# Performance work log

Hardware: AMD Instinct MI355X
Metric: run time of the kernel (lower is better)

The kernel has to match this reference:

```python
import jax, jax.numpy as jnp
import numpy as np

B, L, D, H = 4, 2048, 1024, 16
HD = D // H


def setup_inputs() -> dict:
    key = jax.random.key(0)
    k0, k1, k2, k3, k4 = jax.random.split(key, 5)
    scale = 1.0 / np.sqrt(D)
    x = jax.random.normal(k0, (B, L, D), dtype=jnp.float32)
    Wk = jax.random.normal(k1, (D, D), dtype=jnp.float32) * scale
    Wv = jax.random.normal(k2, (D, D), dtype=jnp.float32) * scale
    Wr = jax.random.normal(k3, (D, D), dtype=jnp.float32) * scale
    Wo = jax.random.normal(k4, (D, D), dtype=jnp.float32) * scale
    # time_decay init: geometric decay per head, broadcast over head_dim
    decay = jnp.exp(-5.0 * jnp.arange(1, H + 1, dtype=jnp.float32) / H)
    time_decay = jnp.broadcast_to(decay[:, None], (H, HD)).astype(jnp.float32)
    time_first = jnp.full((H, HD), 0.5, dtype=jnp.float32)
    return {"x": x, "Wk": Wk, "Wv": Wv, "Wr": Wr, "Wo": Wo,
            "time_decay": time_decay, "time_first": time_first}


def reference(x, Wk, Wv, Wr, Wo, time_decay, time_first):
    b, l, d = x.shape
    h, hd = time_decay.shape
    # projections (nn.Linear: x @ W.T)
    k = (x @ Wk.T).reshape(b, l, h, hd)
    v = (x @ Wv.T).reshape(b, l, h, hd)
    r = jax.nn.sigmoid(x @ Wr.T).reshape(b, l, h, hd)

    decay = time_decay[None, :, :, None]   # (1,H,HD,1) broadcast over 'e' axis
    tf = time_first[None, :, :, None]      # (1,H,HD,1)

    def step(state, inp):
        k_t, v_t, r_t = inp                 # each (B,H,HD)
        # state: (B,H,HD,HD); outer product k_t (d) x v_t (e)
        state = state * decay + (k_t[..., :, None] * v_t[..., None, :]) * tf
        y_t = jnp.einsum('bhde,bhd->bhe', state, r_t)
        return state, y_t

    state0 = jnp.zeros((b, h, hd, hd), dtype=x.dtype)
    seq = (jnp.moveaxis(k, 1, 0), jnp.moveaxis(v, 1, 0), jnp.moveaxis(r, 1, 0))
    final_state, ys = jax.lax.scan(step, state0, seq)   # ys: (L,B,H,HD)
    y = jnp.moveaxis(ys, 0, 1).reshape(b, l, d) @ Wo.T
    return y, final_state
```

## Files before the change

### kernel.cpp

```cpp
#include <hip/hip_runtime.h>

typedef unsigned short u16;
typedef unsigned int   u32;
typedef __attribute__((ext_vector_type(8))) short bfrag;
typedef __attribute__((ext_vector_type(4))) float ffrag;

#define MFMA16(a,b,c) __builtin_amdgcn_mfma_f32_16x16x32_bf16((a),(b),(c),0,0,0)

#define GLL16(gp, lp) __builtin_amdgcn_global_load_lds( \
    (const __attribute__((address_space(1))) u32*)(gp), \
    (__attribute__((address_space(3))) u32*)(lp), 16, 0, 0)

__device__ __forceinline__ u16 f2b(float f) {
  u32 u = __float_as_uint(f);
  return (u16)((u + 0x7fffu + ((u >> 16) & 1u)) >> 16);
}
__device__ __forceinline__ float b2f(u16 v) { return __uint_as_float(((u32)v) << 16); }

__device__ __forceinline__ void unpack8(uint4 q, u16 e[8]) {
  e[0] = q.x & 0xffffu; e[1] = q.x >> 16;
  e[2] = q.y & 0xffffu; e[3] = q.y >> 16;
  e[4] = q.z & 0xffffu; e[5] = q.z >> 16;
  e[6] = q.w & 0xffffu; e[7] = q.w >> 16;
}

__device__ __forceinline__ bfrag scale_frag(bfrag a, float s) {
  u16* p = (u16*)&a;
  bfrag r;
  u16* q = (u16*)&r;
#pragma unroll
  for (int j = 0; j < 8; ++j) q[j] = f2b(b2f(p[j]) * s);
  return r;
}

__global__ __launch_bounds__(256) void cvt_all(
    const float* __restrict__ x,  const float* __restrict__ wk,
    const float* __restrict__ wv, const float* __restrict__ wr,
    const float* __restrict__ wo,
    u16* __restrict__ xb, u16* __restrict__ wb, u16* __restrict__ wob)
{
  size_t i4 = ((size_t)blockIdx.x * 256 + threadIdx.x) * 4;
  const float* src; u16* dst; size_t off;
  if      (i4 <  8388608) { src = x;  dst = xb;            off = i4; }
  else if (i4 <  9437184) { src = wk; dst = wb;            off = i4 - 8388608; }
  else if (i4 < 10485760) { src = wv; dst = wb + 1048576;  off = i4 - 9437184; }
  else if (i4 < 11534336) { src = wr; dst = wb + 2097152;  off = i4 - 10485760; }
  else                    { src = wo; dst = wob;           off = i4 - 11534336; }
  float4 f = *(const float4*)(src + off);
  u16 o[4] = { f2b(f.x), f2b(f.y), f2b(f.z), f2b(f.w) };
  *(ushort4*)(dst + off) = make_ushort4(o[0], o[1], o[2], o[3]);
}

__global__ __launch_bounds__(256) void k1_proj(
    const u16* __restrict__ xb, const u16* __restrict__ wb,
    const float* __restrict__ tf,
    u16* __restrict__ kws, u16* __restrict__ vws, u16* __restrict__ rws)
{
  __shared__ u16 As[2][128 * 32];
  __shared__ u16 Bs[2][128 * 32];
  const int tid  = threadIdx.x;
  const int wave = tid >> 6, lane = tid & 63;
  const int li = lane & 15, quad = lane >> 4;
  const int wr = (wave >> 1) * 64, wc = (wave & 1) * 64;

  const int bid = blockIdx.x;
  const int xcd = bid & 7, lb = bid >> 3;
  const int n0 = (xcd * 3 + (lb % 3)) * 128;
  const int m0 = (lb / 3) * 128;

  ffrag acc[4][4];
#pragma unroll
  for (int i = 0; i < 4; ++i)
#pragma unroll
    for (int j = 0; j < 4; ++j)
#pragma unroll
      for (int r = 0; r < 4; ++r) acc[i][j][r] = 0.f;

  const int srow = wave * 16 + (lane >> 2);
  const int scol = (lane & 3) * 8;

  for (int kk = 0; kk < 1024; kk += 64) {
    const u16* ga = xb + (size_t)(m0 + srow) * 1024 + kk + scol;
    const u16* gb = wb + (size_t)(n0 + srow) * 1024 + kk + scol;
    GLL16(ga,                  As[0] + wave * 512);
    GLL16(ga + 64 * 1024,      As[0] + 2048 + wave * 512);
    GLL16(ga + 32,             As[1] + wave * 512);
    GLL16(ga + 32 + 64 * 1024, As[1] + 2048 + wave * 512);
    GLL16(gb,                  Bs[0] + wave * 512);
    GLL16(gb + 64 * 1024,      Bs[0] + 2048 + wave * 512);
    GLL16(gb + 32,             Bs[1] + wave * 512);
    GLL16(gb + 32 + 64 * 1024, Bs[1] + 2048 + wave * 512);
    __syncthreads();

#pragma unroll
    for (int h2 = 0; h2 < 2; ++h2) {
      bfrag av[4], bv[4];
#pragma unroll
      for (int i = 0; i < 4; ++i) av[i] = *(const bfrag*)&As[h2][(wr + i * 16 + li) * 32 + quad * 8];
#pragma unroll
      for (int j = 0; j < 4; ++j) bv[j] = *(const bfrag*)&Bs[h2][(wc + j * 16 + li) * 32 + quad * 8];
#pragma unroll
      for (int i = 0; i < 4; ++i)
#pragma unroll
        for (int j = 0; j < 4; ++j)
          acc[i][j] = MFMA16(av[i], bv[j], acc[i][j]);
    }
    __syncthreads();
  }

  const int sel = n0 >> 10;
#pragma unroll
  for (int i = 0; i < 4; ++i) {
#pragma unroll
    for (int j = 0; j < 4; ++j) {
#pragma unroll
      for (int r = 0; r < 4; ++r) {
        int m = m0 + wr + i * 16 + quad * 4 + r;
        int n = n0 + wc + j * 16 + li;
        int c = n & 1023;
        int bb = m >> 11, l = m & 2047;
        size_t dst = (size_t)((bb << 4) | (c >> 6)) * 131072 + (size_t)l * 64 + (c & 63);
        float v = acc[i][j][r];
        if (sel == 0)      kws[dst] = f2b(v * tf[c]);
        else if (sel == 1) vws[dst] = f2b(v);
        else               rws[dst] = f2b(1.f / (1.f + __expf(-v)));
      }
    }
  }
}

#define ST 72

__global__ __launch_bounds__(256) void k2a_u(
    const u16* __restrict__ kws, const u16* __restrict__ vws,
    const float* __restrict__ td, float* __restrict__ ut)
{
  __shared__ u16 KbarT[64 * ST];
  __shared__ u16 Vt[64 * ST];
  const int tid = threadIdx.x;
  const int lane = tid & 63, wave = tid >> 6;
  const int li = lane & 15, quad = lane >> 4;
  const int wr = (wave >> 1) * 32, wc = (wave & 1) * 32;
  const int bid = blockIdx.x;
  const int bh = bid >> 5, ch = bid & 31;
  const int h = bh & 15;
  const float l2D = log2f(td[h * 64]);
  const size_t base = (size_t)bh * 131072 + (size_t)ch * 4096;

#pragma unroll
  for (int it = 0; it < 2; ++it) {
    int c16 = tid + it * 256;
    int row = c16 >> 3, c8 = (c16 & 7) * 8;
    size_t g = base + (size_t)row * 64 + c8;
    uint4 kq = *(const uint4*)(kws + g);
    u16 ke[8]; unpack8(kq, ke);
    float sk = exp2f((float)(63 - row) * l2D);
#pragma unroll
    for (int j = 0; j < 8; ++j) KbarT[(c8 + j) * ST + row] = f2b(b2f(ke[j]) * sk);
    uint4 vq = *(const uint4*)(vws + g);
    u16 ve[8]; unpack8(vq, ve);
#pragma unroll
    for (int j = 0; j < 8; ++j) Vt[(c8 + j) * ST + row] = ve[j];
  }
  __syncthreads();

  ffrag U[2][2];
#pragma unroll
  for (int a = 0; a < 2; ++a)
#pragma unroll
    for (int b = 0; b < 2; ++b)
#pragma unroll
      for (int r = 0; r < 4; ++r) U[a][b][r] = 0.f;
#pragma unroll
  for (int kk = 0; kk < 64; kk += 32) {
    bfrag a0 = *(const bfrag*)&Vt[(wr + li) * ST + kk + quad * 8];
    bfrag a1 = *(const bfrag*)&Vt[(wr + 16 + li) * ST + kk + quad * 8];
    bfrag b0 = *(const bfrag*)&KbarT[(wc + li) * ST + kk + quad * 8];
    bfrag b1 = *(const bfrag*)&KbarT[(wc + 16 + li) * ST + kk + quad * 8];
    U[0][0] = MFMA16(a0, b0, U[0][0]);
    U[0][1] = MFMA16(a0, b1, U[0][1]);
    U[1][0] = MFMA16(a1, b0, U[1][0]);
    U[1][1] = MFMA16(a1, b1, U[1][1]);
  }

  float* dst = ut + ((size_t)bid << 12);
#pragma unroll
  for (int ti = 0; ti < 2; ++ti)
#pragma unroll
    for (int tj = 0; tj < 2; ++tj)
#pragma unroll
      for (int r = 0; r < 4; ++r) {
        int e = wr + ti * 16 + quad * 4 + r;
        int d = wc + tj * 16 + li;
        dst[e * 64 + d] = U[ti][tj][r];
      }
}

__global__ __launch_bounds__(256) void k2b_scan(
    const float* __restrict__ ut, const float* __restrict__ td,
    u16* __restrict__ sbf, float* __restrict__ fstate)
{
  __shared__ float Sl[4 * 65];
  const int tid = threadIdx.x;
  const int bid = blockIdx.x;
  const int bh = bid >> 4, q = bid & 15;
  const int ed = q * 256 + tid;
  const int h = bh & 15;
  const float Dh = td[h * 64];
  const float DhC = exp2f(64.f * log2f(Dh));

  float S = 0.f;
  size_t idx = ((size_t)bh * 32) * 4096 + ed;
  for (int c = 0; c < 32; ++c, idx += 4096) {
    sbf[idx] = f2b(S);
    S = S * DhC + ut[idx];
  }
  Sl[(tid >> 6) * 65 + (tid & 63)] = S;
  __syncthreads();
  int d = tid >> 2, el = tid & 3;
  fstate[(size_t)bh * 4096 + (size_t)d * 64 + q * 4 + el] = Sl[el * 65 + d];
}

__global__ __launch_bounds__(256) void k2c_y(
    const u16* __restrict__ kws, const u16* __restrict__ vws, const u16* __restrict__ rws,
    const u16* __restrict__ sbf, const float* __restrict__ td,
    u16* __restrict__ yws)
{
  __shared__ u16 Rc[64 * ST];
  __shared__ u16 KcA[64 * ST];
  __shared__ u16 Vt[64 * ST];
  __shared__ u16 STc[64 * ST];
  __shared__ float Dpow[65];

  const int tid = threadIdx.x;
  const int lane = tid & 63, wave = tid >> 6;
  const int li = lane & 15, quad = lane >> 4;
  const int wr = (wave >> 1) * 32, wc = (wave & 1) * 32;
  const int bid = blockIdx.x;
  const int bh = bid >> 5, ch = bid & 31;
  const int h = bh & 15, bb = bh >> 4;
  const float l2D = log2f(td[h * 64]);
  if (tid <= 64) Dpow[tid] = exp2f((float)tid * l2D);

  const size_t base = (size_t)bh * 131072 + (size_t)ch * 4096;
  const u16* sp = sbf + ((size_t)bid << 12);

#pragma unroll
  for (int it = 0; it < 2; ++it) {
    int c16 = tid + it * 256;
    int row = c16 >> 3, c8 = (c16 & 7) * 8;
    size_t g = base + (size_t)row * 64 + c8;
    *(uint4*)&Rc[row * ST + c8]  = *(const uint4*)(rws + g);
    *(uint4*)&KcA[row * ST + c8] = *(const uint4*)(kws + g);
    *(uint4*)&STc[row * ST + c8] = *(const uint4*)(sp + (size_t)row * 64 + c8);
    uint4 vq = *(const uint4*)(vws + g);
    u16 ve[8]; unpack8(vq, ve);
#pragma unroll
    for (int j = 0; j < 8; ++j) Vt[(c8 + j) * ST + row] = ve[j];
  }
  __syncthreads();

  ffrag P[2][2], Y[2][2];
#pragma unroll
  for (int a = 0; a < 2; ++a)
#pragma unroll
    for (int b = 0; b < 2; ++b)
#pragma unroll
      for (int r = 0; r < 4; ++r) { P[a][b][r] = 0.f; Y[a][b][r] = 0.f; }

  const float sc0 = Dpow[wr + li + 1];
  const float sc1 = Dpow[wr + 16 + li + 1];
#pragma unroll
  for (int kk = 0; kk < 64; kk += 32) {
    bfrag a0 = *(const bfrag*)&Rc[(wr + li) * ST + kk + quad * 8];
    bfrag a1 = *(const bfrag*)&Rc[(wr + 16 + li) * ST + kk + quad * 8];
    bfrag b0 = *(const bfrag*)&KcA[(wc + li) * ST + kk + quad * 8];
    bfrag b1 = *(const bfrag*)&KcA[(wc + 16 + li) * ST + kk + quad * 8];
    P[0][0] = MFMA16(a0, b0, P[0][0]);
    P[0][1] = MFMA16(a0, b1, P[0][1]);
    P[1][0] = MFMA16(a1, b0, P[1][0]);
    P[1][1] = MFMA16(a1, b1, P[1][1]);
    bfrag s0 = *(const bfrag*)&STc[(wc + li) * ST + kk + quad * 8];
    bfrag s1 = *(const bfrag*)&STc[(wc + 16 + li) * ST + kk + quad * 8];
    bfrag as0 = scale_frag(a0, sc0);
    bfrag as1 = scale_frag(a1, sc1);
    Y[0][0] = MFMA16(as0, s0, Y[0][0]);
    Y[0][1] = MFMA16(as0, s1, Y[0][1]);
    Y[1][0] = MFMA16(as1, s0, Y[1][0]);
    Y[1][1] = MFMA16(as1, s1, Y[1][1]);
  }
  __syncthreads();

#pragma unroll
  for (int ti = 0; ti < 2; ++ti)
#pragma unroll
    for (int tj = 0; tj < 2; ++tj)
#pragma unroll
      for (int r = 0; r < 4; ++r) {
        int t = wr + ti * 16 + quad * 4 + r;
        int s = wc + tj * 16 + li;
        float v = (t >= s) ? P[ti][tj][r] * Dpow[t - s] : 0.f;
        KcA[t * ST + s] = f2b(v);
      }
  __syncthreads();

#pragma unroll
  for (int kk = 0; kk < 64; kk += 32) {
    bfrag aa0 = *(const bfrag*)&KcA[(wr + li) * ST + kk + quad * 8];
    bfrag aa1 = *(const bfrag*)&KcA[(wr + 16 + li) * ST + kk + quad * 8];
    bfrag vb0 = *(const bfrag*)&Vt[(wc + li) * ST + kk + quad * 8];
    bfrag vb1 = *(const bfrag*)&Vt[(wc + 16 + li) * ST + kk + quad * 8];
    Y[0][0] = MFMA16(aa0, vb0, Y[0][0]);
    Y[0][1] = MFMA16(aa0, vb1, Y[0][1]);
    Y[1][0] = MFMA16(aa1, vb0, Y[1][0]);
    Y[1][1] = MFMA16(aa1, vb1, Y[1][1]);
  }

#pragma unroll
  for (int ti = 0; ti < 2; ++ti)
#pragma unroll
    for (int tj = 0; tj < 2; ++tj)
#pragma unroll
      for (int r = 0; r < 4; ++r) {
        int t = wr + ti * 16 + quad * 4 + r;
        int e = wc + tj * 16 + li;
        yws[((size_t)(bb * 2048 + ch * 64 + t)) * 1024 + h * 64 + e] = f2b(Y[ti][tj][r]);
      }
}

__global__ __launch_bounds__(256) void k3_out(
    const u16* __restrict__ yb, const u16* __restrict__ wob, float* __restrict__ out)
{
  __shared__ u16 As[2][128 * 32];
  __shared__ u16 Bs[2][128 * 32];
  const int tid  = threadIdx.x;
  const int wave = tid >> 6, lane = tid & 63;
  const int li = lane & 15, quad = lane >> 4;
  const int wr = (wave >> 1) * 64, wc = (wave & 1) * 64;
  const int bid = blockIdx.x;
  const int n0 = (bid & 7) * 128, m0 = (bid >> 3) * 128;

  ffrag acc[4][4];
#pragma unroll
  for (int i = 0; i < 4; ++i)
#pragma unroll
    for (int j = 0; j < 4; ++j)
#pragma unroll
      for (int r = 0; r < 4; ++r) acc[i][j][r] = 0.f;

  const int srow = wave * 16 + (lane >> 2);
  const int scol = (lane & 3) * 8;

  for (int kk = 0; kk < 1024; kk += 64) {
    const u16* ga = yb  + (size_t)(m0 + srow) * 1024 + kk + scol;
    const u16* gb = wob + (size_t)(n0 + srow) * 1024 + kk + scol;
    GLL16(ga,                  As[0] + wave * 512);
    GLL16(ga + 64 * 1024,      As[0] + 2048 + wave * 512);
    GLL16(ga + 32,             As[1] + wave * 512);
    GLL16(ga + 32 + 64 * 1024, As[1] + 2048 + wave * 512);
    GLL16(gb,                  Bs[0] + wave * 512);
    GLL16(gb + 64 * 1024,      Bs[0] + 2048 + wave * 512);
    GLL16(gb + 32,             Bs[1] + wave * 512);
    GLL16(gb + 32 + 64 * 1024, Bs[1] + 2048 + wave * 512);
    __syncthreads();

#pragma unroll
    for (int h2 = 0; h2 < 2; ++h2) {
      bfrag av[4], bv[4];
#pragma unroll
      for (int i = 0; i < 4; ++i) av[i] = *(const bfrag*)&As[h2][(wr + i * 16 + li) * 32 + quad * 8];
#pragma unroll
      for (int j = 0; j < 4; ++j) bv[j] = *(const bfrag*)&Bs[h2][(wc + j * 16 + li) * 32 + quad * 8];
#pragma unroll
      for (int i = 0; i < 4; ++i)
#pragma unroll
        for (int j = 0; j < 4; ++j)
          acc[i][j] = MFMA16(av[i], bv[j], acc[i][j]);
    }
    __syncthreads();
  }

#pragma unroll
  for (int i = 0; i < 4; ++i)
#pragma unroll
    for (int j = 0; j < 4; ++j)
#pragma unroll
      for (int r = 0; r < 4; ++r) {
        int m = m0 + wr + i * 16 + quad * 4 + r;
        int n = n0 + wc + j * 16 + li;
        out[(size_t)m * 1024 + n] = acc[i][j][r];
      }
}

extern "C" void kernel_launch(void* const* d_in, const int* in_sizes, int n_in,
                              void* d_out, int out_size, void* d_ws, size_t ws_size,
                              hipStream_t stream) {
  const float* x  = (const float*)d_in[0];
  const float* Wk = (const float*)d_in[1];
  const float* Wv = (const float*)d_in[2];
  const float* Wr = (const float*)d_in[3];
  const float* Wo = (const float*)d_in[4];
  const float* td = (const float*)d_in[5];
  const float* tf = (const float*)d_in[6];
  float* out = (float*)d_out;

  u16* ws  = (u16*)d_ws;
  u16* xb  = ws;
  u16* wb  = ws + 8388608;
  u16* wob = ws + 11534336;
  u16* kws = ws + 12582912;
  u16* vws = ws + 20971520;
  u16* rws = ws + 29360128;
  float* ut  = (float*)(ws + 37748736);
  u16*   sbf = ws + 54525952;
  u16* yws = xb;

  hipLaunchKernelGGL(cvt_all, dim3(12288), dim3(256), 0, stream,
                     x, Wk, Wv, Wr, Wo, xb, wb, wob);
  hipLaunchKernelGGL(k1_proj, dim3(1536), dim3(256), 0, stream,
                     xb, wb, tf, kws, vws, rws);
  hipLaunchKernelGGL(k2a_u, dim3(2048), dim3(256), 0, stream,
                     kws, vws, td, ut);
  hipLaunchKernelGGL(k2b_scan, dim3(1024), dim3(256), 0, stream,
                     ut, td, sbf, out + 8388608);
  hipLaunchKernelGGL(k2c_y, dim3(2048), dim3(256), 0, stream,
                     kws, vws, rws, sbf, td, yws);
  hipLaunchKernelGGL(k3_out, dim3(512), dim3(256), 0, stream,
                     yws, wob, out);
}
```

Before: 255.5 us.

## Double-buffer GEMM K-loop prefetch, remap tiles per XCD, move decay scaling to accumulators

Both projection GEMMs (k1_proj and k3_out) move from a load-all, sync, compute, sync loop over K=64 chunks to a ping-pong pipeline. The next 32-wide K slice is issued via global_load_lds while the current slice is fed to MFMA, with one barrier per step. Block-to-tile mapping is changed so each XCD handles a contiguous group of M rows, which should improve L2 reuse of the activation rows. In the chunk kernel, the per-row decay scaling of r fragments before MFMA (a bf16 unpack/scale/repack) is replaced by scaling the fp32 Y accumulators afterward. That cuts VALU work and avoids rounding a scaled value back to bf16.

```diff
diff --git a/kernel.cpp b/kernel.cpp
--- a/kernel.cpp
+++ b/kernel.cpp
@@ -22,15 +22,6 @@
   e[2] = q.y & 0xffffu; e[3] = q.y >> 16;
   e[4] = q.z & 0xffffu; e[5] = q.z >> 16;
   e[6] = q.w & 0xffffu; e[7] = q.w >> 16;
-}
-
-__device__ __forceinline__ bfrag scale_frag(bfrag a, float s) {
-  u16* p = (u16*)&a;
-  bfrag r;
-  u16* q = (u16*)&r;
-#pragma unroll
-  for (int j = 0; j < 8; ++j) q[j] = f2b(b2f(p[j]) * s);
-  return r;
 }
 
 __global__ __launch_bounds__(256) void cvt_all(
@@ -64,63 +55,65 @@
   const int wr = (wave >> 1) * 64, wc = (wave & 1) * 64;
 
   const int bid = blockIdx.x;
-  const int xcd = bid & 7, lb = bid >> 3;
-  const int n0 = (xcd * 3 + (lb % 3)) * 128;
-  const int m0 = (lb / 3) * 128;
+  const int xcd = bid & 7, j = bid >> 3;
+  const int n0 = (j >> 3) * 128;
+  const int m0 = ((xcd << 3) | (j & 7)) * 128;
 
   ffrag acc[4][4];
 #pragma unroll
   for (int i = 0; i < 4; ++i)
 #pragma unroll
-    for (int j = 0; j < 4; ++j)
-#pragma unroll
-      for (int r = 0; r < 4; ++r) acc[i][j][r] = 0.f;
+    for (int jj = 0; jj < 4; ++jj)
+#pragma unroll
+      for (int r = 0; r < 4; ++r) acc[i][jj][r] = 0.f;
 
   const int srow = wave * 16 + (lane >> 2);
   const int scol = (lane & 3) * 8;
-
-  for (int kk = 0; kk < 1024; kk += 64) {
-    const u16* ga = xb + (size_t)(m0 + srow) * 1024 + kk + scol;
-    const u16* gb = wb + (size_t)(n0 + srow) * 1024 + kk + scol;
-    GLL16(ga,                  As[0] + wave * 512);
-    GLL16(ga + 64 * 1024,      As[0] + 2048 + wave * 512);
-    GLL16(ga + 32,             As[1] + wave * 512);
-    GLL16(ga + 32 + 64 * 1024, As[1] + 2048 + wave * 512);
-    GLL16(gb,                  Bs[0] + wave * 512);
-    GLL16(gb + 64 * 1024,      Bs[0] + 2048 + wave * 512);
-    GLL16(gb + 32,             Bs[1] + wave * 512);
-    GLL16(gb + 32 + 64 * 1024, Bs[1] + 2048 + wave * 512);
+  const u16* ga0 = xb + (size_t)(m0 + srow) * 1024 + scol;
+  const u16* gb0 = wb + (size_t)(n0 + srow) * 1024 + scol;
+
+  GLL16(ga0,             As[0] + wave * 512);
+  GLL16(ga0 + 64 * 1024, As[0] + 2048 + wave * 512);
+  GLL16(gb0,             Bs[0] + wave * 512);
+  GLL16(gb0 + 64 * 1024, Bs[0] + 2048 + wave * 512);
+
+  for (int it = 0; it < 32; ++it) {
     __syncthreads();
-
-#pragma unroll
-    for (int h2 = 0; h2 < 2; ++h2) {
-      bfrag av[4], bv[4];
-#pragma unroll
-      for (int i = 0; i < 4; ++i) av[i] = *(const bfrag*)&As[h2][(wr + i * 16 + li) * 32 + quad * 8];
-#pragma unroll
-      for (int j = 0; j < 4; ++j) bv[j] = *(const bfrag*)&Bs[h2][(wc + j * 16 + li) * 32 + quad * 8];
-#pragma unroll
-      for (int i = 0; i < 4; ++i)
-#pragma unroll
-        for (int j = 0; j < 4; ++j)
-          acc[i][j] = MFMA16(av[i], bv[j], acc[i][j]);
+    if (it + 1 < 32) {
+      const int nb = (it + 1) & 1;
+      const u16* ga = ga0 + (it + 1) * 32;
+      const u16* gb = gb0 + (it + 1) * 32;
+      GLL16(ga,             As[nb] + wave * 512);
+      GLL16(ga + 64 * 1024, As[nb] + 2048 + wave * 512);
+      GLL16(gb,             Bs[nb] + wave * 512);
+      GLL16(gb + 64 * 1024, Bs[nb] + 2048 + wave * 512);
     }
-    __syncthreads();
+    const int cb = it & 1;
+    bfrag av[4], bv[4];
+#pragma unroll
+    for (int i = 0; i < 4; ++i) av[i] = *(const bfrag*)&As[cb][(wr + i * 16 + li) * 32 + quad * 8];
+#pragma unroll
+    for (int jj = 0; jj < 4; ++jj) bv[jj] = *(const bfrag*)&Bs[cb][(wc + jj * 16 + li) * 32 + quad * 8];
+#pragma unroll
+    for (int i = 0; i < 4; ++i)
+#pragma unroll
+      for (int jj = 0; jj < 4; ++jj)
+        acc[i][jj] = MFMA16(av[i], bv[jj], acc[i][jj]);
   }
 
   const int sel = n0 >> 10;
 #pragma unroll
   for (int i = 0; i < 4; ++i) {
 #pragma unroll
-    for (int j = 0; j < 4; ++j) {
+    for (int jj = 0; jj < 4; ++jj) {
 #pragma unroll
       for (int r = 0; r < 4; ++r) {
         int m = m0 + wr + i * 16 + quad * 4 + r;
-        int n = n0 + wc + j * 16 + li;
+        int n = n0 + wc + jj * 16 + li;
         int c = n & 1023;
         int bb = m >> 11, l = m & 2047;
         size_t dst = (size_t)((bb << 4) | (c >> 6)) * 131072 + (size_t)l * 64 + (c & 63);
-        float v = acc[i][j][r];
+        float v = acc[i][jj][r];
         if (sel == 0)      kws[dst] = f2b(v * tf[c]);
         else if (sel == 1) vws[dst] = f2b(v);
         else               rws[dst] = f2b(1.f / (1.f + __expf(-v)));
@@ -156,11 +149,11 @@
     u16 ke[8]; unpack8(kq, ke);
     float sk = exp2f((float)(63 - row) * l2D);
 #pragma unroll
-    for (int j = 0; j < 8; ++j) KbarT[(c8 + j) * ST + row] = f2b(b2f(ke[j]) * sk);
+    for (int jj = 0; jj < 8; ++jj) KbarT[(c8 + jj) * ST + row] = f2b(b2f(ke[jj]) * sk);
     uint4 vq = *(const uint4*)(vws + g);
     u16 ve[8]; unpack8(vq, ve);
 #pragma unroll
-    for (int j = 0; j < 8; ++j) Vt[(c8 + j) * ST + row] = ve[j];
+    for (int jj = 0; jj < 8; ++jj) Vt[(c8 + jj) * ST + row] = ve[jj];
   }
   __syncthreads();
 
@@ -256,7 +249,7 @@
     uint4 vq = *(const uint4*)(vws + g);
     u16 ve[8]; unpack8(vq, ve);
 #pragma unroll
-    for (int j = 0; j < 8; ++j) Vt[(c8 + j) * ST + row] = ve[j];
+    for (int jj = 0; jj < 8; ++jj) Vt[(c8 + jj) * ST + row] = ve[jj];
   }
   __syncthreads();
 
@@ -268,8 +261,6 @@
 #pragma unroll
       for (int r = 0; r < 4; ++r) { P[a][b][r] = 0.f; Y[a][b][r] = 0.f; }
 
-  const float sc0 = Dpow[wr + li + 1];
-  const float sc1 = Dpow[wr + 16 + li + 1];
 #pragma unroll
   for (int kk = 0; kk < 64; kk += 32) {
     bfrag a0 = *(const bfrag*)&Rc[(wr + li) * ST + kk + quad * 8];
@@ -282,13 +273,21 @@
     P[1][1] = MFMA16(a1, b1, P[1][1]);
     bfrag s0 = *(const bfrag*)&STc[(wc + li) * ST + kk + quad * 8];
     bfrag s1 = *(const bfrag*)&STc[(wc + 16 + li) * ST + kk + quad * 8];
-    bfrag as0 = scale_frag(a0, sc0);
-    bfrag as1 = scale_frag(a1, sc1);
-    Y[0][0] = MFMA16(as0, s0, Y[0][0]);
-    Y[0][1] = MFMA16(as0, s1, Y[0][1]);
-    Y[1][0] = MFMA16(as1, s0, Y[1][0]);
-    Y[1][1] = MFMA16(as1, s1, Y[1][1]);
-  }
+    Y[0][0] = MFMA16(a0, s0, Y[0][0]);
+    Y[0][1] = MFMA16(a0, s1, Y[0][1]);
+    Y[1][0] = MFMA16(a1, s0, Y[1][0]);
+    Y[1][1] = MFMA16(a1, s1, Y[1][1]);
+  }
+
+#pragma unroll
+  for (int ti = 0; ti < 2; ++ti)
+#pragma unroll
+    for (int tj = 0; tj < 2; ++tj)
+#pragma unroll
+      for (int r = 0; r < 4; ++r) {
+        int t = wr + ti * 16 + quad * 4 + r;
+        Y[ti][tj][r] *= Dpow[t + 1];
+      }
   __syncthreads();
 
 #pragma unroll
@@ -338,57 +337,61 @@
   const int li = lane & 15, quad = lane >> 4;
   const int wr = (wave >> 1) * 64, wc = (wave & 1) * 64;
   const int bid = blockIdx.x;
-  const int n0 = (bid & 7) * 128, m0 = (bid >> 3) * 128;
+  const int xcd = bid & 7, j = bid >> 3;
+  const int n0 = (j >> 3) * 128;
+  const int m0 = ((xcd << 3) | (j & 7)) * 128;
 
   ffrag acc[4][4];
 #pragma unroll
   for (int i = 0; i < 4; ++i)
 #pragma unroll
-    for (int j = 0; j < 4; ++j)
-#pragma unroll
-      for (int r = 0; r < 4; ++r) acc[i][j][r] = 0.f;
+    for (int jj = 0; jj < 4; ++jj)
+#pragma unroll
+      for (int r = 0; r < 4; ++r) acc[i][jj][r] = 0.f;
 
   const int srow = wave * 16 + (lane >> 2);
   const int scol = (lane & 3) * 8;
-
-  for (int kk = 0; kk < 1024; kk += 64) {
-    const u16* ga = yb  + (size_t)(m0 + srow) * 1024 + kk + scol;
-    const u16* gb = wob + (size_t)(n0 + srow) * 1024 + kk + scol;
-    GLL16(ga,                  As[0] + wave * 512);
-    GLL16(ga + 64 * 1024,      As[0] + 2048 + wave * 512);
-    GLL16(ga + 32,             As[1] + wave * 512);
-    GLL16(ga + 32 + 64 * 1024, As[1] + 2048 + wave * 512);
-    GLL16(gb,                  Bs[0] + wave * 512);
-    GLL16(gb + 64 * 1024,      Bs[0] + 2048 + wave * 512);
-    GLL16(gb + 32,             Bs[1] + wave * 512);
-    GLL16(gb + 32 + 64 * 1024, Bs[1] + 2048 + wave * 512);
+  const u16* ga0 = yb  + (size_t)(m0 + srow) * 1024 + scol;
+  const u16* gb0 = wob + (size_t)(n0 + srow) * 1024 + scol;
+
+  GLL16(ga0,             As[0] + wave * 512);
+  GLL16(ga0 + 64 * 1024, As[0] + 2048 + wave * 512);
+  GLL16(gb0,             Bs[0] + wave * 512);
+  GLL16(gb0 + 64 * 1024, Bs[0] + 2048 + wave * 512);
+
+  for (int it = 0; it < 32; ++it) {
     __syncthreads();
-
-#pragma unroll
-    for (int h2 = 0; h2 < 2; ++h2) {
-      bfrag av[4], bv[4];
-#pragma unroll
-      for (int i = 0; i < 4; ++i) av[i] = *(const bfrag*)&As[h2][(wr + i * 16 + li) * 32 + quad * 8];
-#pragma unroll
-      for (int j = 0; j < 4; ++j) bv[j] = *(const bfrag*)&Bs[h2][(wc + j * 16 + li) * 32 + quad * 8];
-#pragma unroll
-      for (int i = 0; i < 4; ++i)
-#pragma unroll
-        for (int j = 0; j < 4; ++j)
-          acc[i][j] = MFMA16(av[i], bv[j], acc[i][j]);
+    if (it + 1 < 32) {
+      const int nb = (it + 1) & 1;
+      const u16* ga = ga0 + (it + 1) * 32;
+      const u16* gb = gb0 + (it + 1) * 32;
+      GLL16(ga,             As[nb] + wave * 512);
+      GLL16(ga + 64 * 1024, As[nb] + 2048 + wave * 512);
+      GLL16(gb,             Bs[nb] + wave * 512);
+      GLL16(gb + 64 * 1024, Bs[nb] + 2048 + wave * 512);
     }
-    __syncthreads();
+    const int cb = it & 1;
+    bfrag av[4], bv[4];
+#pragma unroll
+    for (int i = 0; i < 4; ++i) av[i] = *(const bfrag*)&As[cb][(wr + i * 16 + li) * 32 + quad * 8];
+#pragma unroll
+    for (int jj = 0; jj < 4; ++jj) bv[jj] = *(const bfrag*)&Bs[cb][(wc + jj * 16 + li) * 32 + quad * 8];
+#pragma unroll
+    for (int i = 0; i < 4; ++i)
+#pragma unroll
+      for (int jj = 0; jj < 4; ++jj)
+        acc[i][jj] = MFMA16(av[i], bv[jj], acc[i][jj]);
   }
 
 #pragma unroll
   for (int i = 0; i < 4; ++i)
 #pragma unroll
-    for (int j = 0; j < 4; ++j)
+    for (int jj = 0; jj < 4; ++jj)
 #pragma unroll
       for (int r = 0; r < 4; ++r) {
         int m = m0 + wr + i * 16 + quad * 4 + r;
-        int n = n0 + wc + j * 16 + li;
-        out[(size_t)m * 1024 + n] = acc[i][j][r];
+        int n = n0 + wc + jj * 16 + li;
+        out[(size_t)m * 1024 + n] = acc[i][jj][r];
       }
 }
 
```

Result: faster. 250.1 us (-2.1%).
